# Performance work log

Hardware: AMD Instinct MI355X
Metric: run time of the kernel (lower is better)

## Reference

```python
import jax, jax.numpy as jnp
import numpy as np

B, S, D, H = 2, 2048, 1024, 16
DK = D // H
THETA = 10000.0


def apply_rope(t, pos):
    # t: [B, H, S, DK], pos: [B, S] int
    half = DK // 2
    inv_freq = THETA ** (-jnp.arange(0, DK, 2, dtype=jnp.float32) / DK)  # [half]
    ang = pos.astype(jnp.float32)[:, None, :, None] * inv_freq  # [B,1,S,half]
    cos, sin = jnp.cos(ang), jnp.sin(ang)
    t1, t2 = t[..., 0::2], t[..., 1::2]  # interleaved pairs
    r1 = t1 * cos - t2 * sin
    r2 = t1 * sin + t2 * cos
    return jnp.stack([r1, r2], axis=-1).reshape(t.shape)


def setup_inputs() -> dict:
    key = jax.random.key(0)
    ks = jax.random.split(key, 5)
    x = jax.random.normal(ks[0], (B, S, D), dtype=jnp.float32)
    scale = 0.02
    Wq = jax.random.normal(ks[1], (D, D), dtype=jnp.float32) * scale
    Wk = jax.random.normal(ks[2], (D, D), dtype=jnp.float32) * scale
    Wv = jax.random.normal(ks[3], (D, D), dtype=jnp.float32) * scale
    Wo = jax.random.normal(ks[4], (D, D), dtype=jnp.float32) * scale
    token_positions = jnp.broadcast_to(jnp.arange(S, dtype=jnp.int64), (B, S))
    return {"x": x, "Wq": Wq, "Wk": Wk, "Wv": Wv, "Wo": Wo,
            "token_positions": token_positions}


def reference(x, Wq, Wk, Wv, Wo, token_positions):
    # Bias-free linear projections: y = x @ W^T (torch Linear convention)
    q = jnp.einsum('bsd,ed->bse', x, Wq)
    k = jnp.einsum('bsd,ed->bse', x, Wk)
    v = jnp.einsum('bsd,ed->bse', x, Wv)
    # split heads: [B, S, H*DK] -> [B, H, S, DK]
    def split(t):
        return t.reshape(B, S, H, DK).transpose(0, 2, 1, 3)
    qh, kh, vh = split(q), split(k), split(v)
    qh = apply_rope(qh, token_positions)
    kh = apply_rope(kh, token_positions)
    scores = jnp.einsum('bhqd,bhkd->bhqk', qh, kh) / jnp.sqrt(jnp.float32(DK))
    causal = jnp.tril(jnp.ones((S, S), dtype=bool))
    scores = jnp.where(causal, scores, jnp.finfo(scores.dtype).min)
    probs = jax.nn.softmax(scores, axis=-1)
    out = jnp.einsum('bhqk,bhkd->bhqd', probs, vh)  # [B,H,S,DK]
    out = out.transpose(0, 2, 1, 3).reshape(B, S, D)
    return jnp.einsum('bsd,ed->bse', out, Wo)
```

## Files before the change

### kernel.cpp

```cpp
#include <hip/hip_runtime.h>
#include <stdint.h>

#define B_  2
#define S_  2048
#define D_  1024
#define H_  16
#define DK_ 64

using bf16x8 = __attribute__((ext_vector_type(8))) short;
using f32x4  = __attribute__((ext_vector_type(4))) float;

__device__ __forceinline__ unsigned short f2bf(float f) {
    union { float f; uint32_t u; } v; v.f = f;
    uint32_t r = v.u + 0x7FFFu + ((v.u >> 16) & 1u);
    return (unsigned short)(r >> 16);
}

__device__ __forceinline__ uint32_t cvtpk(float lo, float hi) {
    uint32_t r;
    asm("v_cvt_pk_bf16_f32 %0, %1, %2" : "=v"(r) : "v"(lo), "v"(hi));
    return r;
}
__device__ __forceinline__ void ps32(uint32_t& a, uint32_t& b) {
    asm volatile("v_permlane32_swap_b32 %0, %1" : "+v"(a), "+v"(b));
}
__device__ __forceinline__ void ps16(uint32_t& a, uint32_t& b) {
    asm volatile("v_permlane16_swap_b32 %0, %1" : "+v"(a), "+v"(b));
}

#define GLD16(G, L) __builtin_amdgcn_global_load_lds( \
    (const __attribute__((address_space(1))) void*)(const void*)(G), \
    (__attribute__((address_space(3))) void*)(void*)(L), 16, 0, 0)

__global__ __launch_bounds__(256) void k_f32_to_bf16(const float* __restrict__ src,
                                                     unsigned short* __restrict__ dst,
                                                     int n4) {
    int i = blockIdx.x * 256 + threadIdx.x;
    if (i >= n4) return;
    float4 v = ((const float4*)src)[i];
    union { unsigned short u[4]; uint2 d; } o;
    o.u[0] = f2bf(v.x); o.u[1] = f2bf(v.y); o.u[2] = f2bf(v.z); o.u[3] = f2bf(v.w);
    ((uint2*)dst)[i] = o.d;
}

__global__ __launch_bounds__(256) void k_wconv(
    const float* __restrict__ s0, const float* __restrict__ s1,
    const float* __restrict__ s2, const float* __restrict__ s3,
    unsigned short* __restrict__ d0, unsigned short* __restrict__ d1,
    unsigned short* __restrict__ d2, unsigned short* __restrict__ d3) {
    const int w = blockIdx.y;
    const float* s = w == 0 ? s0 : w == 1 ? s1 : w == 2 ? s2 : s3;
    unsigned short* d = w == 0 ? d0 : w == 1 ? d1 : w == 2 ? d2 : d3;
    int i = blockIdx.x * 256 + threadIdx.x;
    float4 v = ((const float4*)s)[i];
    union { unsigned short u[4]; uint2 dd; } o;
    o.u[0] = f2bf(v.x); o.u[1] = f2bf(v.y); o.u[2] = f2bf(v.z); o.u[3] = f2bf(v.w);
    ((uint2*)d)[i] = o.dd;
}

template<int MODE>
__global__ __launch_bounds__(256) void k_gemm_bt(
    const unsigned short* __restrict__ A,
    const unsigned short* __restrict__ W0,
    const unsigned short* __restrict__ W1,
    const unsigned short* __restrict__ W2,
    void* __restrict__ C0, void* __restrict__ C1, void* __restrict__ C2,
    int M, int N, int K)
{
    __shared__ __align__(16) unsigned short As[2][128 * 32];
    __shared__ __align__(16) unsigned short Bs[2][128 * 32];

    const int tid  = threadIdx.x;
    const int wid  = tid >> 6, lane = tid & 63;
    const int m16  = lane & 15, g = lane >> 4;
    const int m0   = blockIdx.x * 128, n0 = blockIdx.y * 128;
    const unsigned short* Wm = blockIdx.z == 0 ? W0 : (blockIdx.z == 1 ? W1 : W2);
    void* Cm = blockIdx.z == 0 ? C0 : (blockIdx.z == 1 ? C1 : C2);

    const int wm = (wid >> 1) * 64, wn = (wid & 1) * 64;
    const int srow = lane >> 2;
    const int scol = ((lane & 3) ^ ((lane >> 3) & 3)) * 8;
    const int sw8  = (m16 >> 1) & 3;

    const f32x4 fz = {0.f, 0.f, 0.f, 0.f};
    f32x4 acc[4][4];
#pragma unroll
    for (int i = 0; i < 4; ++i)
#pragma unroll
        for (int j = 0; j < 4; ++j) acc[i][j] = fz;

#pragma unroll
    for (int c = 0; c < 2; ++c) {
        const int chunk = wid * 2 + c;
        const int row   = chunk * 16 + srow;
        GLD16(A  + (size_t)(m0 + row) * K + scol, &As[0][chunk * 512]);
        GLD16(Wm + (size_t)(n0 + row) * K + scol, &Bs[0][chunk * 512]);
    }
    __syncthreads();

    int buf = 0;
    for (int k0 = 0; k0 < K; k0 += 32) {
        if (k0 + 32 < K) {
#pragma unroll
            for (int c = 0; c < 2; ++c) {
                const int chunk = wid * 2 + c;
                const int row   = chunk * 16 + srow;
                GLD16(A  + (size_t)(m0 + row) * K + k0 + 32 + scol, &As[buf ^ 1][chunk * 512]);
                GLD16(Wm + (size_t)(n0 + row) * K + k0 + 32 + scol, &Bs[buf ^ 1][chunk * 512]);
            }
        }
        bf16x8 af[4], bf[4];
#pragma unroll
        for (int i = 0; i < 4; ++i)
            af[i] = *(const bf16x8*)(&As[buf][(wm + i * 16 + m16) * 32 + ((g ^ sw8) * 8)]);
#pragma unroll
        for (int j = 0; j < 4; ++j)
            bf[j] = *(const bf16x8*)(&Bs[buf][(wn + j * 16 + m16) * 32 + ((g ^ sw8) * 8)]);
#pragma unroll
        for (int i = 0; i < 4; ++i)
#pragma unroll
            for (int j = 0; j < 4; ++j)
                acc[i][j] = __builtin_amdgcn_mfma_f32_16x16x32_bf16(af[i], bf[j], acc[i][j], 0, 0, 0);
        __syncthreads();
        buf ^= 1;
    }

#pragma unroll
    for (int i = 0; i < 4; ++i) {
#pragma unroll
        for (int j = 0; j < 4; ++j) {
#pragma unroll
            for (int r = 0; r < 4; ++r) {
                const int row = m0 + wm + i * 16 + g * 4 + r;
                const int col = n0 + wn + j * 16 + m16;
                const float val = acc[i][j][r];
                if (MODE == 1) {
                    ((float*)Cm)[(size_t)row * N + col] = val;
                } else {
                    const int b = row >> 11, s = row & (S_ - 1);
                    const int h = col >> 6,  dk = col & (DK_ - 1);
                    size_t idx;
                    if (blockIdx.z == 2)
                        idx = ((size_t)((b * H_ + h) * DK_ + dk)) * S_ + s;
                    else
                        idx = ((size_t)((b * H_ + h) * S_ + s)) * DK_ + dk;
                    ((unsigned short*)Cm)[idx] = f2bf(val);
                }
            }
        }
    }
}

__global__ __launch_bounds__(256) void k_rope_inplace(
    unsigned short* __restrict__ qh, unsigned short* __restrict__ kh,
    const int* __restrict__ tok)
{
    const int idx = blockIdx.x * 256 + threadIdx.x;
    const int c = idx & 7;
    const int s = (idx >> 3) & (S_ - 1);
    const int b = idx >> 18;
    const size_t off = (size_t)idx * 8;

    const float pos = (float)tok[b * S_ + s];
    float cs[4], sn[4];
#pragma unroll
    for (int i = 0; i < 4; ++i) {
        const int p = c * 4 + i;
        const float inv = exp2f((float)(-2 * p) * (13.287712379549449f / 64.f));
        sincosf(pos * inv, &sn[i], &cs[i]);
    }
    bf16x8 qv = *(bf16x8*)(qh + off);
    bf16x8 kv = *(bf16x8*)(kh + off);
    bf16x8 qo, ko;
#pragma unroll
    for (int i = 0; i < 4; ++i) {
        union { uint32_t u; float f; } q1{(uint32_t)(unsigned short)qv[2*i] << 16};
        union { uint32_t u; float f; } q2{(uint32_t)(unsigned short)qv[2*i+1] << 16};
        qo[2 * i]     = (short)f2bf(q1.f * cs[i] - q2.f * sn[i]);
        qo[2 * i + 1] = (short)f2bf(q1.f * sn[i] + q2.f * cs[i]);
        union { uint32_t u; float f; } k1{(uint32_t)(unsigned short)kv[2*i] << 16};
        union { uint32_t u; float f; } k2{(uint32_t)(unsigned short)kv[2*i+1] << 16};
        ko[2 * i]     = (short)f2bf(k1.f * cs[i] - k2.f * sn[i]);
        ko[2 * i + 1] = (short)f2bf(k1.f * sn[i] + k2.f * cs[i]);
    }
    *(bf16x8*)(qh + off) = qo;
    *(bf16x8*)(kh + off) = ko;
}

__global__ __launch_bounds__(256, 2) void k_fattn6(
    const unsigned short* __restrict__ Q,
    const unsigned short* __restrict__ K,
    const unsigned short* __restrict__ Vt,
    unsigned short* __restrict__ O)
{
    __shared__ __align__(16) unsigned short Ks[2][64 * 64];
    __shared__ __align__(16) unsigned short Vs[2][64 * 64];

    const int tid = threadIdx.x, wid = tid >> 6, lane = tid & 63;
    const int m16 = lane & 15, g = lane >> 4;
    const int bh = blockIdx.x & 31;
    const int j  = blockIdx.x >> 5;
    const int b = bh >> 4, h = bh & 15;
    const unsigned short* Qb = Q  + (size_t)bh * S_ * DK_;
    const unsigned short* Kb = K  + (size_t)bh * S_ * DK_;
    const unsigned short* Vb = Vt + (size_t)bh * DK_ * S_;

    const int r8   = lane >> 3;
    const int slot = (lane & 7) ^ r8;
    const int ch0  = wid * 2, ch1 = wid * 2 + 1;

    const f32x4 fz = {0.f, 0.f, 0.f, 0.f};
    const float kSc = 0.125f * 1.4426950408889634f;

    GLD16(Kb + (size_t)(ch0 * 8 + r8) * DK_ + slot * 8, &Ks[0][ch0 * 512]);
    GLD16(Kb + (size_t)(ch1 * 8 + r8) * DK_ + slot * 8, &Ks[0][ch1 * 512]);
    GLD16(Vb + (size_t)(ch0 * 8 + r8) * S_  + slot * 8, &Vs[0][ch0 * 512]);
    GLD16(Vb + (size_t)(ch1 * 8 + r8) * S_  + slot * 8, &Vs[0][ch1 * 512]);
    __syncthreads();

    int buf = 0;
#pragma unroll
    for (int ph = 0; ph < 2; ++ph) {
        const int qi = ph ? 31 - j : j;
        const int q0 = qi * 64;
        const int qw0 = q0 + wid * 16;

        bf16x8 qf[2];
        {
            const unsigned short* qp = Qb + (size_t)(qw0 + m16) * DK_ + g * 8;
            qf[0] = *(const bf16x8*)(qp);
            qf[1] = *(const bf16x8*)(qp + 32);
        }

        f32x4 o[4];
#pragma unroll
        for (int i = 0; i < 4; ++i) o[i] = fz;
        float ps = 0.f;

        const int nt = qi + 1;
        for (int t = 0; t < nt; ++t) {
            const int kv0 = t * 64;
            int nkv0 = -1;
            if (t + 1 < nt)      nkv0 = kv0 + 64;
            else if (ph == 0)    nkv0 = 0;
            if (nkv0 >= 0) {
                GLD16(Kb + (size_t)(nkv0 + ch0 * 8 + r8) * DK_ + slot * 8, &Ks[buf ^ 1][ch0 * 512]);
                GLD16(Kb + (size_t)(nkv0 + ch1 * 8 + r8) * DK_ + slot * 8, &Ks[buf ^ 1][ch1 * 512]);
                GLD16(Vb + (size_t)(ch0 * 8 + r8) * S_ + nkv0 + slot * 8, &Vs[buf ^ 1][ch0 * 512]);
                GLD16(Vb + (size_t)(ch1 * 8 + r8) * S_ + nkv0 + slot * 8, &Vs[buf ^ 1][ch1 * 512]);
            }

            f32x4 sc[4];
            __builtin_amdgcn_s_setprio(1);
#pragma unroll
            for (int c = 0; c < 4; ++c) {
                const int row = c * 16 + m16, rr = row & 7;
                bf16x8 kf0 = *(const bf16x8*)(&Ks[buf][row * 64 + ((g ^ rr) << 3)]);
                bf16x8 kf1 = *(const bf16x8*)(&Ks[buf][row * 64 + (((4 + g) ^ rr) << 3)]);
                f32x4 z = fz;
                z = __builtin_amdgcn_mfma_f32_16x16x32_bf16(kf0, qf[0], z, 0, 0, 0);
                z = __builtin_amdgcn_mfma_f32_16x16x32_bf16(kf1, qf[1], z, 0, 0, 0);
                sc[c] = z;
            }
            __builtin_amdgcn_s_setprio(0);

            bf16x8 vf[2][4];
#pragma unroll
            for (int c2 = 0; c2 < 4; ++c2) {
                const int rv = (c2 * 16 + m16) & 7;
                vf[0][c2] = *(const bf16x8*)(&Vs[buf][(c2 * 16 + m16) * 64 + ((g ^ rv) << 3)]);
                vf[1][c2] = *(const bf16x8*)(&Vs[buf][(c2 * 16 + m16) * 64 + (((4 + g) ^ rv) << 3)]);
            }

            const bool maskT = (t == qi);
            const int qrow = qw0 + m16;
            uint32_t pk[4][2];
#pragma unroll
            for (int c = 0; c < 4; ++c) {
                float p[4];
#pragma unroll
                for (int r = 0; r < 4; ++r) {
                    float v = exp2f(sc[c][r] * kSc);
                    if (maskT && (kv0 + c * 16 + g * 4 + r > qrow)) v = 0.f;
                    p[r] = v;
                }
                ps += (p[0] + p[1]) + (p[2] + p[3]);
                pk[c][0] = cvtpk(p[0], p[1]);
                pk[c][1] = cvtpk(p[2], p[3]);
            }

            bf16x8 pf[2];
#pragma unroll
            for (int ks = 0; ks < 2; ++ks) {
                uint32_t ylo = pk[2 * ks][0], zlo = pk[2 * ks + 1][0];
                ps32(ylo, zlo); ps16(ylo, zlo);
                uint32_t yhi = pk[2 * ks][1], zhi = pk[2 * ks + 1][1];
                ps32(yhi, zhi); ps16(yhi, zhi);
                union { uint32_t u[4]; bf16x8 v; } fu;
                fu.u[0] = ylo; fu.u[1] = yhi; fu.u[2] = zlo; fu.u[3] = zhi;
                pf[ks] = fu.v;
            }

            __builtin_amdgcn_s_setprio(1);
#pragma unroll
            for (int c2 = 0; c2 < 4; ++c2) {
                o[c2] = __builtin_amdgcn_mfma_f32_16x16x32_bf16(pf[0], vf[0][c2], o[c2], 0, 0, 0);
                o[c2] = __builtin_amdgcn_mfma_f32_16x16x32_bf16(pf[1], vf[1][c2], o[c2], 0, 0, 0);
            }
            __builtin_amdgcn_s_setprio(0);

            __syncthreads();
            buf ^= 1;
        }

        float s = ps;
        s += __shfl_xor(s, 16);
        s += __shfl_xor(s, 32);
        const float inv = 1.f / s;
        float lrq[4];
#pragma unroll
        for (int r = 0; r < 4; ++r)
            lrq[r] = __shfl(inv, g * 4 + r);
#pragma unroll
        for (int c2 = 0; c2 < 4; ++c2)
#pragma unroll
            for (int r = 0; r < 4; ++r) {
                const int orow = qw0 + g * 4 + r;
                const int ocol = h * DK_ + c2 * 16 + m16;
                O[((size_t)(b * S_ + orow)) * D_ + ocol] = f2bf(o[c2][r] * lrq[r]);
            }
    }
}

extern "C" void kernel_launch(void* const* d_in, const int* in_sizes, int n_in,
                              void* d_out, int out_size, void* d_ws, size_t ws_size,
                              hipStream_t stream) {
    (void)in_sizes; (void)n_in; (void)out_size; (void)ws_size;
    const float* x   = (const float*)d_in[0];
    const float* Wq  = (const float*)d_in[1];
    const float* Wk  = (const float*)d_in[2];
    const float* Wv  = (const float*)d_in[3];
    const float* Wo  = (const float*)d_in[4];
    const int*   tok = (const int*)d_in[5];

    char* ws = (char*)d_ws;
    const size_t MB = 1u << 20;
    unsigned short* xb  = (unsigned short*)(ws + 0 * MB);
    unsigned short* wqb = (unsigned short*)(ws + 8 * MB);
    unsigned short* wkb = (unsigned short*)(ws + 10 * MB);
    unsigned short* wvb = (unsigned short*)(ws + 12 * MB);
    unsigned short* wob = (unsigned short*)(ws + 14 * MB);
    unsigned short* qh  = (unsigned short*)(ws + 16 * MB);
    unsigned short* kh  = (unsigned short*)(ws + 24 * MB);
    unsigned short* vh  = (unsigned short*)(ws + 32 * MB);
    unsigned short* ao  = (unsigned short*)(ws + 40 * MB);

    k_f32_to_bf16<<<4096, 256, 0, stream>>>(x, xb, (B_ * S_ * D_) / 4);
    k_wconv<<<dim3(1024, 4), 256, 0, stream>>>(Wq, Wk, Wv, Wo, wqb, wkb, wvb, wob);

    k_gemm_bt<0><<<dim3(32, 8, 3), 256, 0, stream>>>(
        xb, wqb, wkb, wvb, qh, kh, vh, B_ * S_, D_, D_);

    k_rope_inplace<<<2048, 256, 0, stream>>>(qh, kh, tok);

    k_fattn6<<<dim3(512), 256, 0, stream>>>(qh, kh, vh, ao);

    k_gemm_bt<1><<<dim3(32, 8, 1), 256, 0, stream>>>(
        ao, wob, wob, wob, d_out, d_out, d_out, B_ * S_, D_, D_);
}
```

Measured before the change: 122.6 us.

## Split attention warps across query pairs and KV halves with LDS reduction

Changes the warp decomposition in the flash-attention kernel. Each pair of warps now owns 32 query rows, and each warp in the pair handles one 32-column half of every KV tile, so Q fragments and K/V fragment loads are reused across two query sub-tiles. Warps skip KV halves that lie entirely above the causal diagonal. Partial outputs and row sums are combined through shared memory before normalisation, which adds extra LDS traffic, an extra barrier and more registers per warp.

```diff
diff --git a/kernel.cpp b/kernel.cpp
--- a/kernel.cpp
+++ b/kernel.cpp
@@ -187,7 +187,7 @@
     *(bf16x8*)(kh + off) = ko;
 }
 
-__global__ __launch_bounds__(256, 2) void k_fattn6(
+__global__ __launch_bounds__(256, 2) void k_fattn7(
     const unsigned short* __restrict__ Q,
     const unsigned short* __restrict__ K,
     const unsigned short* __restrict__ Vt,
@@ -195,12 +195,16 @@
 {
     __shared__ __align__(16) unsigned short Ks[2][64 * 64];
     __shared__ __align__(16) unsigned short Vs[2][64 * 64];
+    __shared__ __align__(16) f32x4 Cx[2][8][64];
+    __shared__ float Cps[2][2][64];
 
     const int tid = threadIdx.x, wid = tid >> 6, lane = tid & 63;
     const int m16 = lane & 15, g = lane >> 4;
+    const int sub = wid >> 1;
+    const int hf  = wid & 1;
     const int bh = blockIdx.x & 31;
     const int j  = blockIdx.x >> 5;
-    const int b = bh >> 4, h = bh & 15;
+    const int b = bh >> 4, hd = bh & 15;
     const unsigned short* Qb = Q  + (size_t)bh * S_ * DK_;
     const unsigned short* Kb = K  + (size_t)bh * S_ * DK_;
     const unsigned short* Vb = Vt + (size_t)bh * DK_ * S_;
@@ -222,26 +226,27 @@
 #pragma unroll
     for (int ph = 0; ph < 2; ++ph) {
         const int qi = ph ? 31 - j : j;
-        const int q0 = qi * 64;
-        const int qw0 = q0 + wid * 16;
-
-        bf16x8 qf[2];
-        {
-            const unsigned short* qp = Qb + (size_t)(qw0 + m16) * DK_ + g * 8;
-            qf[0] = *(const bf16x8*)(qp);
-            qf[1] = *(const bf16x8*)(qp + 32);
-        }
-
-        f32x4 o[4];
-#pragma unroll
-        for (int i = 0; i < 4; ++i) o[i] = fz;
-        float ps = 0.f;
-
-        const int nt = qi + 1;
-        for (int t = 0; t < nt; ++t) {
-            const int kv0 = t * 64;
+        const int qw0 = qi * 64 + sub * 32;
+
+        bf16x8 qf[2][2];
+#pragma unroll
+        for (int mi = 0; mi < 2; ++mi) {
+            const unsigned short* qp = Qb + (size_t)(qw0 + mi * 16 + m16) * DK_ + g * 8;
+            qf[mi][0] = *(const bf16x8*)(qp);
+            qf[mi][1] = *(const bf16x8*)(qp + 32);
+        }
+
+        f32x4 o[2][4];
+#pragma unroll
+        for (int mi = 0; mi < 2; ++mi)
+#pragma unroll
+            for (int i = 0; i < 4; ++i) o[mi][i] = fz;
+        float psum[2] = {0.f, 0.f};
+
+        const int S = qi + 1;
+        for (int s = 0; s < S; ++s) {
             int nkv0 = -1;
-            if (t + 1 < nt)      nkv0 = kv0 + 64;
+            if (s + 1 < S)       nkv0 = (s + 1) * 64;
             else if (ph == 0)    nkv0 = 0;
             if (nkv0 >= 0) {
                 GLD16(Kb + (size_t)(nkv0 + ch0 * 8 + r8) * DK_ + slot * 8, &Ks[buf ^ 1][ch0 * 512]);
@@ -250,85 +255,110 @@
                 GLD16(Vb + (size_t)(ch1 * 8 + r8) * S_ + nkv0 + slot * 8, &Vs[buf ^ 1][ch1 * 512]);
             }
 
-            f32x4 sc[4];
-            __builtin_amdgcn_s_setprio(1);
-#pragma unroll
-            for (int c = 0; c < 4; ++c) {
-                const int row = c * 16 + m16, rr = row & 7;
-                bf16x8 kf0 = *(const bf16x8*)(&Ks[buf][row * 64 + ((g ^ rr) << 3)]);
-                bf16x8 kf1 = *(const bf16x8*)(&Ks[buf][row * 64 + (((4 + g) ^ rr) << 3)]);
-                f32x4 z = fz;
-                z = __builtin_amdgcn_mfma_f32_16x16x32_bf16(kf0, qf[0], z, 0, 0, 0);
-                z = __builtin_amdgcn_mfma_f32_16x16x32_bf16(kf1, qf[1], z, 0, 0, 0);
-                sc[c] = z;
+            const int kvb = s * 64 + hf * 32;
+            if (kvb <= qw0 + 31) {
+                bf16x8 kf[2][2];
+#pragma unroll
+                for (int cc = 0; cc < 2; ++cc) {
+                    const int row = (2 * hf + cc) * 16 + m16, rr = row & 7;
+                    kf[cc][0] = *(const bf16x8*)(&Ks[buf][row * 64 + ((g ^ rr) << 3)]);
+                    kf[cc][1] = *(const bf16x8*)(&Ks[buf][row * 64 + (((4 + g) ^ rr) << 3)]);
+                }
+                f32x4 sc[2][2];
+                __builtin_amdgcn_s_setprio(1);
+#pragma unroll
+                for (int cc = 0; cc < 2; ++cc)
+#pragma unroll
+                    for (int mi = 0; mi < 2; ++mi) {
+                        f32x4 z = fz;
+                        z = __builtin_amdgcn_mfma_f32_16x16x32_bf16(kf[cc][0], qf[mi][0], z, 0, 0, 0);
+                        z = __builtin_amdgcn_mfma_f32_16x16x32_bf16(kf[cc][1], qf[mi][1], z, 0, 0, 0);
+                        sc[mi][cc] = z;
+                    }
+                __builtin_amdgcn_s_setprio(0);
+
+                bf16x8 vf[4];
+#pragma unroll
+                for (int c2 = 0; c2 < 4; ++c2) {
+                    const int dv = c2 * 16 + m16, rv = dv & 7;
+                    vf[c2] = *(const bf16x8*)(&Vs[buf][dv * 64 + (((4 * hf + g) ^ rv) << 3)]);
+                }
+
+                bf16x8 pf[2];
+#pragma unroll
+                for (int mi = 0; mi < 2; ++mi) {
+                    const int qrow = qw0 + mi * 16 + m16;
+                    const bool maskT = (kvb + 31 > qw0 + mi * 16);
+                    uint32_t pkc[2][2];
+#pragma unroll
+                    for (int cc = 0; cc < 2; ++cc) {
+                        float p[4];
+#pragma unroll
+                        for (int r = 0; r < 4; ++r) {
+                            float v = exp2f(sc[mi][cc][r] * kSc);
+                            if (maskT && (kvb + cc * 16 + g * 4 + r > qrow)) v = 0.f;
+                            p[r] = v;
+                        }
+                        psum[mi] += (p[0] + p[1]) + (p[2] + p[3]);
+                        pkc[cc][0] = cvtpk(p[0], p[1]);
+                        pkc[cc][1] = cvtpk(p[2], p[3]);
+                    }
+                    uint32_t ylo = pkc[0][0], zlo = pkc[1][0];
+                    ps32(ylo, zlo); ps16(ylo, zlo);
+                    uint32_t yhi = pkc[0][1], zhi = pkc[1][1];
+                    ps32(yhi, zhi); ps16(yhi, zhi);
+                    union { uint32_t u[4]; bf16x8 v; } fu;
+                    fu.u[0] = ylo; fu.u[1] = yhi; fu.u[2] = zlo; fu.u[3] = zhi;
+                    pf[mi] = fu.v;
+                }
+
+                __builtin_amdgcn_s_setprio(1);
+#pragma unroll
+                for (int mi = 0; mi < 2; ++mi)
+#pragma unroll
+                    for (int c2 = 0; c2 < 4; ++c2)
+                        o[mi][c2] = __builtin_amdgcn_mfma_f32_16x16x32_bf16(pf[mi], vf[c2], o[mi][c2], 0, 0, 0);
+                __builtin_amdgcn_s_setprio(0);
             }
-            __builtin_amdgcn_s_setprio(0);
-
-            bf16x8 vf[2][4];
-#pragma unroll
-            for (int c2 = 0; c2 < 4; ++c2) {
-                const int rv = (c2 * 16 + m16) & 7;
-                vf[0][c2] = *(const bf16x8*)(&Vs[buf][(c2 * 16 + m16) * 64 + ((g ^ rv) << 3)]);
-                vf[1][c2] = *(const bf16x8*)(&Vs[buf][(c2 * 16 + m16) * 64 + (((4 + g) ^ rv) << 3)]);
-            }
-
-            const bool maskT = (t == qi);
-            const int qrow = qw0 + m16;
-            uint32_t pk[4][2];
-#pragma unroll
-            for (int c = 0; c < 4; ++c) {
-                float p[4];
-#pragma unroll
-                for (int r = 0; r < 4; ++r) {
-                    float v = exp2f(sc[c][r] * kSc);
-                    if (maskT && (kv0 + c * 16 + g * 4 + r > qrow)) v = 0.f;
-                    p[r] = v;
-                }
-                ps += (p[0] + p[1]) + (p[2] + p[3]);
-                pk[c][0] = cvtpk(p[0], p[1]);
-                pk[c][1] = cvtpk(p[2], p[3]);
-            }
-
-            bf16x8 pf[2];
-#pragma unroll
-            for (int ks = 0; ks < 2; ++ks) {
-                uint32_t ylo = pk[2 * ks][0], zlo = pk[2 * ks + 1][0];
-                ps32(ylo, zlo); ps16(ylo, zlo);
-                uint32_t yhi = pk[2 * ks][1], zhi = pk[2 * ks + 1][1];
-                ps32(yhi, zhi); ps16(yhi, zhi);
-                union { uint32_t u[4]; bf16x8 v; } fu;
-                fu.u[0] = ylo; fu.u[1] = yhi; fu.u[2] = zlo; fu.u[3] = zhi;
-                pf[ks] = fu.v;
-            }
-
-            __builtin_amdgcn_s_setprio(1);
-#pragma unroll
-            for (int c2 = 0; c2 < 4; ++c2) {
-                o[c2] = __builtin_amdgcn_mfma_f32_16x16x32_bf16(pf[0], vf[0][c2], o[c2], 0, 0, 0);
-                o[c2] = __builtin_amdgcn_mfma_f32_16x16x32_bf16(pf[1], vf[1][c2], o[c2], 0, 0, 0);
-            }
-            __builtin_amdgcn_s_setprio(0);
-
             __syncthreads();
             buf ^= 1;
         }
 
-        float s = ps;
-        s += __shfl_xor(s, 16);
-        s += __shfl_xor(s, 32);
-        const float inv = 1.f / s;
-        float lrq[4];
-#pragma unroll
-        for (int r = 0; r < 4; ++r)
-            lrq[r] = __shfl(inv, g * 4 + r);
-#pragma unroll
-        for (int c2 = 0; c2 < 4; ++c2)
-#pragma unroll
-            for (int r = 0; r < 4; ++r) {
-                const int orow = qw0 + g * 4 + r;
-                const int ocol = h * DK_ + c2 * 16 + m16;
-                O[((size_t)(b * S_ + orow)) * D_ + ocol] = f2bf(o[c2][r] * lrq[r]);
+        if (hf == 1) {
+#pragma unroll
+            for (int mi = 0; mi < 2; ++mi)
+#pragma unroll
+                for (int c2 = 0; c2 < 4; ++c2)
+                    Cx[sub][mi * 4 + c2][lane] = o[mi][c2];
+            Cps[sub][0][lane] = psum[0];
+            Cps[sub][1][lane] = psum[1];
+        }
+        __syncthreads();
+        if (hf == 0) {
+#pragma unroll
+            for (int mi = 0; mi < 2; ++mi) {
+#pragma unroll
+                for (int c2 = 0; c2 < 4; ++c2)
+                    o[mi][c2] += Cx[sub][mi * 4 + c2][lane];
+                float ssum = psum[mi] + Cps[sub][mi][lane];
+                ssum += __shfl_xor(ssum, 16);
+                ssum += __shfl_xor(ssum, 32);
+                const float inv = 1.f / ssum;
+                float lrq[4];
+#pragma unroll
+                for (int r = 0; r < 4; ++r)
+                    lrq[r] = __shfl(inv, g * 4 + r);
+#pragma unroll
+                for (int c2 = 0; c2 < 4; ++c2)
+#pragma unroll
+                    for (int r = 0; r < 4; ++r) {
+                        const int orow = qw0 + mi * 16 + g * 4 + r;
+                        const int ocol = hd * DK_ + c2 * 16 + m16;
+                        O[((size_t)(b * S_ + orow)) * D_ + ocol] = f2bf(o[mi][c2][r] * lrq[r]);
+                    }
             }
+        }
+        __syncthreads();
     }
 }
 
@@ -363,7 +393,7 @@
 
     k_rope_inplace<<<2048, 256, 0, stream>>>(qh, kh, tok);
 
-    k_fattn6<<<dim3(512), 256, 0, stream>>>(qh, kh, vh, ao);
+    k_fattn7<<<dim3(512), 256, 0, stream>>>(qh, kh, vh, ao);
 
     k_gemm_bt<1><<<dim3(32, 8, 1), 256, 0, stream>>>(
         ao, wob, wob, wob, d_out, d_out, d_out, B_ * S_, D_, D_);
```

After: 127.3 us. +3.8%, slower.

## Triple-buffer K/V tiles and fuse both causal phases into one flat loop

Applied to the files above, without the earlier changes.

The attention kernel now keeps three LDS buffers for K/V tiles and prefetches two tiles ahead. It replaces the two-phase nested loop with a single 33-iteration loop that handles both the low and high query tiles, flushing the first output partway through. A single barrier per iteration, placed after an explicit vmcnt wait, replaces the trailing __syncthreads, so the load for the next tile can overlap compute. In exchange, LDS use grows by half, which may limit occupancy, and the manual waitcnt counts must exactly match the number of outstanding loads.

```diff
diff --git a/kernel.cpp b/kernel.cpp
--- a/kernel.cpp
+++ b/kernel.cpp
@@ -187,14 +187,14 @@
     *(bf16x8*)(kh + off) = ko;
 }
 
-__global__ __launch_bounds__(256, 2) void k_fattn6(
+__global__ __launch_bounds__(256, 2) void k_fattn8(
     const unsigned short* __restrict__ Q,
     const unsigned short* __restrict__ K,
     const unsigned short* __restrict__ Vt,
     unsigned short* __restrict__ O)
 {
-    __shared__ __align__(16) unsigned short Ks[2][64 * 64];
-    __shared__ __align__(16) unsigned short Vs[2][64 * 64];
+    __shared__ __align__(16) unsigned short Ks[3][64 * 64];
+    __shared__ __align__(16) unsigned short Vs[3][64 * 64];
 
     const int tid = threadIdx.x, wid = tid >> 6, lane = tid & 63;
     const int m16 = lane & 15, g = lane >> 4;
@@ -211,108 +211,146 @@
 
     const f32x4 fz = {0.f, 0.f, 0.f, 0.f};
     const float kSc = 0.125f * 1.4426950408889634f;
-
-    GLD16(Kb + (size_t)(ch0 * 8 + r8) * DK_ + slot * 8, &Ks[0][ch0 * 512]);
-    GLD16(Kb + (size_t)(ch1 * 8 + r8) * DK_ + slot * 8, &Ks[0][ch1 * 512]);
-    GLD16(Vb + (size_t)(ch0 * 8 + r8) * S_  + slot * 8, &Vs[0][ch0 * 512]);
-    GLD16(Vb + (size_t)(ch1 * 8 + r8) * S_  + slot * 8, &Vs[0][ch1 * 512]);
-    __syncthreads();
-
-    int buf = 0;
-#pragma unroll
-    for (int ph = 0; ph < 2; ++ph) {
-        const int qi = ph ? 31 - j : j;
-        const int q0 = qi * 64;
-        const int qw0 = q0 + wid * 16;
-
-        bf16x8 qf[2];
-        {
-            const unsigned short* qp = Qb + (size_t)(qw0 + m16) * DK_ + g * 8;
-            qf[0] = *(const bf16x8*)(qp);
-            qf[1] = *(const bf16x8*)(qp + 32);
-        }
-
-        f32x4 o[4];
-#pragma unroll
-        for (int i = 0; i < 4; ++i) o[i] = fz;
-        float ps = 0.f;
-
-        const int nt = qi + 1;
-        for (int t = 0; t < nt; ++t) {
-            const int kv0 = t * 64;
-            int nkv0 = -1;
-            if (t + 1 < nt)      nkv0 = kv0 + 64;
-            else if (ph == 0)    nkv0 = 0;
-            if (nkv0 >= 0) {
-                GLD16(Kb + (size_t)(nkv0 + ch0 * 8 + r8) * DK_ + slot * 8, &Ks[buf ^ 1][ch0 * 512]);
-                GLD16(Kb + (size_t)(nkv0 + ch1 * 8 + r8) * DK_ + slot * 8, &Ks[buf ^ 1][ch1 * 512]);
-                GLD16(Vb + (size_t)(ch0 * 8 + r8) * S_ + nkv0 + slot * 8, &Vs[buf ^ 1][ch0 * 512]);
-                GLD16(Vb + (size_t)(ch1 * 8 + r8) * S_ + nkv0 + slot * 8, &Vs[buf ^ 1][ch1 * 512]);
+    const int nt0 = j + 1;
+
+    const int qrow0 = j * 64 + wid * 16 + m16;
+    const int qrow1 = (31 - j) * 64 + wid * 16 + m16;
+    bf16x8 qf0[2], qf1[2];
+    {
+        const unsigned short* qp = Qb + (size_t)qrow0 * DK_ + g * 8;
+        qf0[0] = *(const bf16x8*)(qp);
+        qf0[1] = *(const bf16x8*)(qp + 32);
+    }
+    {
+        const unsigned short* qp = Qb + (size_t)qrow1 * DK_ + g * 8;
+        qf1[0] = *(const bf16x8*)(qp);
+        qf1[1] = *(const bf16x8*)(qp + 32);
+    }
+
+    {
+        GLD16(Kb + (size_t)(ch0 * 8 + r8) * DK_ + slot * 8, &Ks[0][ch0 * 512]);
+        GLD16(Kb + (size_t)(ch1 * 8 + r8) * DK_ + slot * 8, &Ks[0][ch1 * 512]);
+        GLD16(Vb + (size_t)(ch0 * 8 + r8) * S_  + slot * 8, &Vs[0][ch0 * 512]);
+        GLD16(Vb + (size_t)(ch1 * 8 + r8) * S_  + slot * 8, &Vs[0][ch1 * 512]);
+        const int kv1 = (1 < nt0 ? 1 : 0) * 64;
+        GLD16(Kb + (size_t)(kv1 + ch0 * 8 + r8) * DK_ + slot * 8, &Ks[1][ch0 * 512]);
+        GLD16(Kb + (size_t)(kv1 + ch1 * 8 + r8) * DK_ + slot * 8, &Ks[1][ch1 * 512]);
+        GLD16(Vb + (size_t)(ch0 * 8 + r8) * S_ + kv1 + slot * 8, &Vs[1][ch0 * 512]);
+        GLD16(Vb + (size_t)(ch1 * 8 + r8) * S_ + kv1 + slot * 8, &Vs[1][ch1 * 512]);
+    }
+
+    f32x4 o[4];
+#pragma unroll
+    for (int i = 0; i < 4; ++i) o[i] = fz;
+    float ps = 0.f;
+
+    for (int u = 0; u < 33; ++u) {
+        const int phase = (u >= nt0) ? 1 : 0;
+
+        if (u == nt0) {
+            float s = ps;
+            s += __shfl_xor(s, 16);
+            s += __shfl_xor(s, 32);
+            const float inv = 1.f / s;
+            float lrq[4];
+#pragma unroll
+            for (int r = 0; r < 4; ++r)
+                lrq[r] = __shfl(inv, g * 4 + r);
+#pragma unroll
+            for (int c2 = 0; c2 < 4; ++c2)
+#pragma unroll
+                for (int r = 0; r < 4; ++r) {
+                    const int orow = j * 64 + wid * 16 + g * 4 + r;
+                    const int ocol = h * DK_ + c2 * 16 + m16;
+                    O[((size_t)(b * S_ + orow)) * D_ + ocol] = f2bf(o[c2][r] * lrq[r]);
+                }
+#pragma unroll
+            for (int i = 0; i < 4; ++i) o[i] = fz;
+            ps = 0.f;
+        }
+
+        if (u < 32) asm volatile("s_waitcnt vmcnt(4)" ::: "memory");
+        else        asm volatile("s_waitcnt vmcnt(0)" ::: "memory");
+        __builtin_amdgcn_s_barrier();
+        __builtin_amdgcn_sched_barrier(0);
+
+        if (u + 2 < 33) {
+            const int v2 = u + 2;
+            const int kv2 = (v2 < nt0 ? v2 : v2 - nt0) * 64;
+            unsigned short* kd = &Ks[(u + 2) % 3][0];
+            unsigned short* vd = &Vs[(u + 2) % 3][0];
+            GLD16(Kb + (size_t)(kv2 + ch0 * 8 + r8) * DK_ + slot * 8, kd + ch0 * 512);
+            GLD16(Kb + (size_t)(kv2 + ch1 * 8 + r8) * DK_ + slot * 8, kd + ch1 * 512);
+            GLD16(Vb + (size_t)(ch0 * 8 + r8) * S_ + kv2 + slot * 8, vd + ch0 * 512);
+            GLD16(Vb + (size_t)(ch1 * 8 + r8) * S_ + kv2 + slot * 8, vd + ch1 * 512);
+        }
+
+        const int kv0 = (phase ? u - nt0 : u) * 64;
+        const unsigned short* Kbuf = &Ks[u % 3][0];
+        const unsigned short* Vbuf = &Vs[u % 3][0];
+        const bf16x8* qf = phase ? qf1 : qf0;
+        const int qrow = phase ? qrow1 : qrow0;
+
+        f32x4 sc[4];
+        __builtin_amdgcn_s_setprio(1);
+#pragma unroll
+        for (int c = 0; c < 4; ++c) {
+            const int row = c * 16 + m16, rr = row & 7;
+            bf16x8 kf0 = *(const bf16x8*)(Kbuf + row * 64 + ((g ^ rr) << 3));
+            bf16x8 kf1 = *(const bf16x8*)(Kbuf + row * 64 + (((4 + g) ^ rr) << 3));
+            f32x4 z = fz;
+            z = __builtin_amdgcn_mfma_f32_16x16x32_bf16(kf0, qf[0], z, 0, 0, 0);
+            z = __builtin_amdgcn_mfma_f32_16x16x32_bf16(kf1, qf[1], z, 0, 0, 0);
+            sc[c] = z;
+        }
+        __builtin_amdgcn_s_setprio(0);
+
+        bf16x8 vf[2][4];
+#pragma unroll
+        for (int c2 = 0; c2 < 4; ++c2) {
+            const int rv = (c2 * 16 + m16) & 7;
+            vf[0][c2] = *(const bf16x8*)(Vbuf + (c2 * 16 + m16) * 64 + ((g ^ rv) << 3));
+            vf[1][c2] = *(const bf16x8*)(Vbuf + (c2 * 16 + m16) * 64 + (((4 + g) ^ rv) << 3));
+        }
+
+        const bool maskT = (u == nt0 - 1) || (u == 32);
+        uint32_t pk[4][2];
+#pragma unroll
+        for (int c = 0; c < 4; ++c) {
+            float p[4];
+#pragma unroll
+            for (int r = 0; r < 4; ++r) {
+                float v = exp2f(sc[c][r] * kSc);
+                if (maskT && (kv0 + c * 16 + g * 4 + r > qrow)) v = 0.f;
+                p[r] = v;
             }
-
-            f32x4 sc[4];
-            __builtin_amdgcn_s_setprio(1);
-#pragma unroll
-            for (int c = 0; c < 4; ++c) {
-                const int row = c * 16 + m16, rr = row & 7;
-                bf16x8 kf0 = *(const bf16x8*)(&Ks[buf][row * 64 + ((g ^ rr) << 3)]);
-                bf16x8 kf1 = *(const bf16x8*)(&Ks[buf][row * 64 + (((4 + g) ^ rr) << 3)]);
-                f32x4 z = fz;
-                z = __builtin_amdgcn_mfma_f32_16x16x32_bf16(kf0, qf[0], z, 0, 0, 0);
-                z = __builtin_amdgcn_mfma_f32_16x16x32_bf16(kf1, qf[1], z, 0, 0, 0);
-                sc[c] = z;
-            }
-            __builtin_amdgcn_s_setprio(0);
-
-            bf16x8 vf[2][4];
-#pragma unroll
-            for (int c2 = 0; c2 < 4; ++c2) {
-                const int rv = (c2 * 16 + m16) & 7;
-                vf[0][c2] = *(const bf16x8*)(&Vs[buf][(c2 * 16 + m16) * 64 + ((g ^ rv) << 3)]);
-                vf[1][c2] = *(const bf16x8*)(&Vs[buf][(c2 * 16 + m16) * 64 + (((4 + g) ^ rv) << 3)]);
-            }
-
-            const bool maskT = (t == qi);
-            const int qrow = qw0 + m16;
-            uint32_t pk[4][2];
-#pragma unroll
-            for (int c = 0; c < 4; ++c) {
-                float p[4];
-#pragma unroll
-                for (int r = 0; r < 4; ++r) {
-                    float v = exp2f(sc[c][r] * kSc);
-                    if (maskT && (kv0 + c * 16 + g * 4 + r > qrow)) v = 0.f;
-                    p[r] = v;
-                }
-                ps += (p[0] + p[1]) + (p[2] + p[3]);
-                pk[c][0] = cvtpk(p[0], p[1]);
-                pk[c][1] = cvtpk(p[2], p[3]);
-            }
-
-            bf16x8 pf[2];
-#pragma unroll
-            for (int ks = 0; ks < 2; ++ks) {
-                uint32_t ylo = pk[2 * ks][0], zlo = pk[2 * ks + 1][0];
-                ps32(ylo, zlo); ps16(ylo, zlo);
-                uint32_t yhi = pk[2 * ks][1], zhi = pk[2 * ks + 1][1];
-                ps32(yhi, zhi); ps16(yhi, zhi);
-                union { uint32_t u[4]; bf16x8 v; } fu;
-                fu.u[0] = ylo; fu.u[1] = yhi; fu.u[2] = zlo; fu.u[3] = zhi;
-                pf[ks] = fu.v;
-            }
-
-            __builtin_amdgcn_s_setprio(1);
-#pragma unroll
-            for (int c2 = 0; c2 < 4; ++c2) {
-                o[c2] = __builtin_amdgcn_mfma_f32_16x16x32_bf16(pf[0], vf[0][c2], o[c2], 0, 0, 0);
-                o[c2] = __builtin_amdgcn_mfma_f32_16x16x32_bf16(pf[1], vf[1][c2], o[c2], 0, 0, 0);
-            }
-            __builtin_amdgcn_s_setprio(0);
-
-            __syncthreads();
-            buf ^= 1;
-        }
-
+            ps += (p[0] + p[1]) + (p[2] + p[3]);
+            pk[c][0] = cvtpk(p[0], p[1]);
+            pk[c][1] = cvtpk(p[2], p[3]);
+        }
+
+        bf16x8 pf[2];
+#pragma unroll
+        for (int ks = 0; ks < 2; ++ks) {
+            uint32_t ylo = pk[2 * ks][0], zlo = pk[2 * ks + 1][0];
+            ps32(ylo, zlo); ps16(ylo, zlo);
+            uint32_t yhi = pk[2 * ks][1], zhi = pk[2 * ks + 1][1];
+            ps32(yhi, zhi); ps16(yhi, zhi);
+            union { uint32_t u[4]; bf16x8 v; } fu;
+            fu.u[0] = ylo; fu.u[1] = yhi; fu.u[2] = zlo; fu.u[3] = zhi;
+            pf[ks] = fu.v;
+        }
+
+        __builtin_amdgcn_s_setprio(1);
+#pragma unroll
+        for (int c2 = 0; c2 < 4; ++c2) {
+            o[c2] = __builtin_amdgcn_mfma_f32_16x16x32_bf16(pf[0], vf[0][c2], o[c2], 0, 0, 0);
+            o[c2] = __builtin_amdgcn_mfma_f32_16x16x32_bf16(pf[1], vf[1][c2], o[c2], 0, 0, 0);
+        }
+        __builtin_amdgcn_s_setprio(0);
+    }
+
+    {
         float s = ps;
         s += __shfl_xor(s, 16);
         s += __shfl_xor(s, 32);
@@ -325,7 +363,7 @@
         for (int c2 = 0; c2 < 4; ++c2)
 #pragma unroll
             for (int r = 0; r < 4; ++r) {
-                const int orow = qw0 + g * 4 + r;
+                const int orow = (31 - j) * 64 + wid * 16 + g * 4 + r;
                 const int ocol = h * DK_ + c2 * 16 + m16;
                 O[((size_t)(b * S_ + orow)) * D_ + ocol] = f2bf(o[c2][r] * lrq[r]);
             }
@@ -363,7 +401,7 @@
 
     k_rope_inplace<<<2048, 256, 0, stream>>>(qh, kh, tok);
 
-    k_fattn6<<<dim3(512), 256, 0, stream>>>(qh, kh, vh, ao);
+    k_fattn8<<<dim3(512), 256, 0, stream>>>(qh, kh, vh, ao);
 
     k_gemm_bt<1><<<dim3(32, 8, 1), 256, 0, stream>>>(
         ao, wob, wob, wob, d_out, d_out, d_out, B_ * S_, D_, D_);
```

Measured after the change: 128.4 us. 4.8% more time.

## Process two 64-key tiles per barrier in flash attention with 128-wide staging

Applied to the files above, without the earlier changes.

The attention kernel now stages 128 keys of K and V per double-buffered step and computes two 64-key tiles between each barrier, halving the number of __syncthreads and global-load issue rounds. The V staging layout and its swizzle change to a 128-wide row. Shared memory per block doubles to 64 KB, which may limit how many blocks fit per CU. Odd tile counts are handled by skipping the second tile.

```diff
diff --git a/kernel.cpp b/kernel.cpp
--- a/kernel.cpp
+++ b/kernel.cpp
@@ -187,14 +187,81 @@
     *(bf16x8*)(kh + off) = ko;
 }
 
-__global__ __launch_bounds__(256, 2) void k_fattn6(
+#define TILE_PF(T, diag, kvb, pfOut)                                         \
+  {                                                                          \
+    f32x4 sc_[4];                                                            \
+    __builtin_amdgcn_s_setprio(1);                                           \
+    _Pragma("unroll")                                                        \
+    for (int c = 0; c < 4; ++c) {                                            \
+      const int row_ = (T) * 64 + c * 16 + m16, rr_ = row_ & 7;              \
+      bf16x8 kf0 = *(const bf16x8*)(Kbuf + row_ * 64 + ((g ^ rr_) << 3));    \
+      bf16x8 kf1 = *(const bf16x8*)(Kbuf + row_ * 64 + (((4 + g) ^ rr_) << 3)); \
+      f32x4 z_ = fz;                                                         \
+      z_ = __builtin_amdgcn_mfma_f32_16x16x32_bf16(kf0, qf[0], z_, 0, 0, 0); \
+      z_ = __builtin_amdgcn_mfma_f32_16x16x32_bf16(kf1, qf[1], z_, 0, 0, 0); \
+      sc_[c] = z_;                                                           \
+    }                                                                        \
+    __builtin_amdgcn_s_setprio(0);                                           \
+    uint32_t pk_[4][2];                                                      \
+    _Pragma("unroll")                                                        \
+    for (int c = 0; c < 4; ++c) {                                            \
+      float p_[4];                                                           \
+      _Pragma("unroll")                                                      \
+      for (int r = 0; r < 4; ++r) {                                          \
+        float v_ = exp2f(sc_[c][r] * kSc);                                   \
+        if ((diag) && ((kvb) + c * 16 + g * 4 + r > qrow)) v_ = 0.f;         \
+        p_[r] = v_;                                                          \
+      }                                                                      \
+      ps += (p_[0] + p_[1]) + (p_[2] + p_[3]);                               \
+      pk_[c][0] = cvtpk(p_[0], p_[1]);                                       \
+      pk_[c][1] = cvtpk(p_[2], p_[3]);                                       \
+    }                                                                        \
+    _Pragma("unroll")                                                        \
+    for (int ks = 0; ks < 2; ++ks) {                                         \
+      uint32_t ylo = pk_[2 * ks][0], zlo = pk_[2 * ks + 1][0];               \
+      ps32(ylo, zlo); ps16(ylo, zlo);                                        \
+      uint32_t yhi = pk_[2 * ks][1], zhi = pk_[2 * ks + 1][1];               \
+      ps32(yhi, zhi); ps16(yhi, zhi);                                        \
+      union { uint32_t u[4]; bf16x8 v; } fu_;                                \
+      fu_.u[0] = ylo; fu_.u[1] = yhi; fu_.u[2] = zlo; fu_.u[3] = zhi;        \
+      pfOut[ks] = fu_.v;                                                     \
+    }                                                                        \
+  }
+
+#define TILE_PV(T, pfIn)                                                     \
+  {                                                                          \
+    __builtin_amdgcn_s_setprio(1);                                           \
+    _Pragma("unroll")                                                        \
+    for (int c2 = 0; c2 < 4; ++c2) {                                         \
+      const int dv_ = c2 * 16 + m16, rv_ = dv_ & 7;                          \
+      bf16x8 v0 = *(const bf16x8*)(Vbuf + dv_ * 128 + ((((T) * 8 + g) ^ rv_) << 3)); \
+      bf16x8 v1 = *(const bf16x8*)(Vbuf + dv_ * 128 + ((((T) * 8 + 4 + g) ^ rv_) << 3)); \
+      o[c2] = __builtin_amdgcn_mfma_f32_16x16x32_bf16(pfIn[0], v0, o[c2], 0, 0, 0); \
+      o[c2] = __builtin_amdgcn_mfma_f32_16x16x32_bf16(pfIn[1], v1, o[c2], 0, 0, 0); \
+    }                                                                        \
+    __builtin_amdgcn_s_setprio(0);                                           \
+  }
+
+#define STAGE_KV(bd, kb)                                                     \
+  {                                                                          \
+    _Pragma("unroll")                                                        \
+    for (int c = 0; c < 4; ++c) {                                            \
+      const int chunk_ = wid * 4 + c;                                        \
+      const int krow_ = chunk_ * 8 + kr8;                                    \
+      GLD16(Kb + (size_t)((kb) + krow_) * DK_ + kslot * 8, &Ks[bd][chunk_ * 512]); \
+      const int dv_ = chunk_ * 4 + vr4;                                      \
+      GLD16(Vb + (size_t)dv_ * S_ + (kb) + ((vs0 ^ (dv_ & 7)) * 8), &Vs[bd][chunk_ * 512]); \
+    }                                                                        \
+  }
+
+__global__ __launch_bounds__(256, 2) void k_fattn9(
     const unsigned short* __restrict__ Q,
     const unsigned short* __restrict__ K,
     const unsigned short* __restrict__ Vt,
     unsigned short* __restrict__ O)
 {
-    __shared__ __align__(16) unsigned short Ks[2][64 * 64];
-    __shared__ __align__(16) unsigned short Vs[2][64 * 64];
+    __shared__ __align__(16) unsigned short Ks[2][128 * 64];
+    __shared__ __align__(16) unsigned short Vs[2][64 * 128];
 
     const int tid = threadIdx.x, wid = tid >> 6, lane = tid & 63;
     const int m16 = lane & 15, g = lane >> 4;
@@ -205,29 +272,27 @@
     const unsigned short* Kb = K  + (size_t)bh * S_ * DK_;
     const unsigned short* Vb = Vt + (size_t)bh * DK_ * S_;
 
-    const int r8   = lane >> 3;
-    const int slot = (lane & 7) ^ r8;
-    const int ch0  = wid * 2, ch1 = wid * 2 + 1;
+    const int kr8 = lane >> 3;
+    const int kslot = (lane & 7) ^ kr8;
+    const int vr4 = lane >> 4;
+    const int vs0 = lane & 15;
 
     const f32x4 fz = {0.f, 0.f, 0.f, 0.f};
     const float kSc = 0.125f * 1.4426950408889634f;
 
-    GLD16(Kb + (size_t)(ch0 * 8 + r8) * DK_ + slot * 8, &Ks[0][ch0 * 512]);
-    GLD16(Kb + (size_t)(ch1 * 8 + r8) * DK_ + slot * 8, &Ks[0][ch1 * 512]);
-    GLD16(Vb + (size_t)(ch0 * 8 + r8) * S_  + slot * 8, &Vs[0][ch0 * 512]);
-    GLD16(Vb + (size_t)(ch1 * 8 + r8) * S_  + slot * 8, &Vs[0][ch1 * 512]);
+    STAGE_KV(0, 0)
     __syncthreads();
 
     int buf = 0;
 #pragma unroll
     for (int ph = 0; ph < 2; ++ph) {
         const int qi = ph ? 31 - j : j;
-        const int q0 = qi * 64;
-        const int qw0 = q0 + wid * 16;
+        const int qw0 = qi * 64 + wid * 16;
+        const int qrow = qw0 + m16;
 
         bf16x8 qf[2];
         {
-            const unsigned short* qp = Qb + (size_t)(qw0 + m16) * DK_ + g * 8;
+            const unsigned short* qp = Qb + (size_t)qrow * DK_ + g * 8;
             qf[0] = *(const bf16x8*)(qp);
             qf[1] = *(const bf16x8*)(qp + 32);
         }
@@ -238,76 +303,25 @@
         float ps = 0.f;
 
         const int nt = qi + 1;
-        for (int t = 0; t < nt; ++t) {
-            const int kv0 = t * 64;
-            int nkv0 = -1;
-            if (t + 1 < nt)      nkv0 = kv0 + 64;
-            else if (ph == 0)    nkv0 = 0;
-            if (nkv0 >= 0) {
-                GLD16(Kb + (size_t)(nkv0 + ch0 * 8 + r8) * DK_ + slot * 8, &Ks[buf ^ 1][ch0 * 512]);
-                GLD16(Kb + (size_t)(nkv0 + ch1 * 8 + r8) * DK_ + slot * 8, &Ks[buf ^ 1][ch1 * 512]);
-                GLD16(Vb + (size_t)(ch0 * 8 + r8) * S_ + nkv0 + slot * 8, &Vs[buf ^ 1][ch0 * 512]);
-                GLD16(Vb + (size_t)(ch1 * 8 + r8) * S_ + nkv0 + slot * 8, &Vs[buf ^ 1][ch1 * 512]);
-            }
-
-            f32x4 sc[4];
-            __builtin_amdgcn_s_setprio(1);
-#pragma unroll
-            for (int c = 0; c < 4; ++c) {
-                const int row = c * 16 + m16, rr = row & 7;
-                bf16x8 kf0 = *(const bf16x8*)(&Ks[buf][row * 64 + ((g ^ rr) << 3)]);
-                bf16x8 kf1 = *(const bf16x8*)(&Ks[buf][row * 64 + (((4 + g) ^ rr) << 3)]);
-                f32x4 z = fz;
-                z = __builtin_amdgcn_mfma_f32_16x16x32_bf16(kf0, qf[0], z, 0, 0, 0);
-                z = __builtin_amdgcn_mfma_f32_16x16x32_bf16(kf1, qf[1], z, 0, 0, 0);
-                sc[c] = z;
-            }
-            __builtin_amdgcn_s_setprio(0);
-
-            bf16x8 vf[2][4];
-#pragma unroll
-            for (int c2 = 0; c2 < 4; ++c2) {
-                const int rv = (c2 * 16 + m16) & 7;
-                vf[0][c2] = *(const bf16x8*)(&Vs[buf][(c2 * 16 + m16) * 64 + ((g ^ rv) << 3)]);
-                vf[1][c2] = *(const bf16x8*)(&Vs[buf][(c2 * 16 + m16) * 64 + (((4 + g) ^ rv) << 3)]);
-            }
-
-            const bool maskT = (t == qi);
-            const int qrow = qw0 + m16;
-            uint32_t pk[4][2];
-#pragma unroll
-            for (int c = 0; c < 4; ++c) {
-                float p[4];
-#pragma unroll
-                for (int r = 0; r < 4; ++r) {
-                    float v = exp2f(sc[c][r] * kSc);
-                    if (maskT && (kv0 + c * 16 + g * 4 + r > qrow)) v = 0.f;
-                    p[r] = v;
-                }
-                ps += (p[0] + p[1]) + (p[2] + p[3]);
-                pk[c][0] = cvtpk(p[0], p[1]);
-                pk[c][1] = cvtpk(p[2], p[3]);
-            }
-
-            bf16x8 pf[2];
-#pragma unroll
-            for (int ks = 0; ks < 2; ++ks) {
-                uint32_t ylo = pk[2 * ks][0], zlo = pk[2 * ks + 1][0];
-                ps32(ylo, zlo); ps16(ylo, zlo);
-                uint32_t yhi = pk[2 * ks][1], zhi = pk[2 * ks + 1][1];
-                ps32(yhi, zhi); ps16(yhi, zhi);
-                union { uint32_t u[4]; bf16x8 v; } fu;
-                fu.u[0] = ylo; fu.u[1] = yhi; fu.u[2] = zlo; fu.u[3] = zhi;
-                pf[ks] = fu.v;
-            }
-
-            __builtin_amdgcn_s_setprio(1);
-#pragma unroll
-            for (int c2 = 0; c2 < 4; ++c2) {
-                o[c2] = __builtin_amdgcn_mfma_f32_16x16x32_bf16(pf[0], vf[0][c2], o[c2], 0, 0, 0);
-                o[c2] = __builtin_amdgcn_mfma_f32_16x16x32_bf16(pf[1], vf[1][c2], o[c2], 0, 0, 0);
-            }
-            __builtin_amdgcn_s_setprio(0);
+        const int nI = (nt + 1) >> 1;
+        for (int i = 0; i < nI; ++i) {
+            int nkb = -1;
+            if (i + 1 < nI)      nkb = (i + 1) * 128;
+            else if (ph == 0)    nkb = 0;
+            if (nkb >= 0) STAGE_KV(buf ^ 1, nkb)
+
+            const unsigned short* Kbuf = Ks[buf];
+            const unsigned short* Vbuf = Vs[buf];
+            const int kbA = i * 128;
+            const bool vB = (2 * i + 1 < nt);
+            const bool dA = (2 * i == nt - 1);
+            const bool dB = (2 * i + 1 == nt - 1);
+
+            bf16x8 pfA[2], pfB[2];
+            TILE_PF(0, dA, kbA, pfA)
+            if (vB) { TILE_PF(1, dB, kbA + 64, pfB) }
+            TILE_PV(0, pfA)
+            if (vB) { TILE_PV(1, pfB) }
 
             __syncthreads();
             buf ^= 1;
@@ -363,7 +377,7 @@
 
     k_rope_inplace<<<2048, 256, 0, stream>>>(qh, kh, tok);
 
-    k_fattn6<<<dim3(512), 256, 0, stream>>>(qh, kh, vh, ao);
+    k_fattn9<<<dim3(512), 256, 0, stream>>>(qh, kh, vh, ao);
 
     k_gemm_bt<1><<<dim3(32, 8, 1), 256, 0, stream>>>(
         ao, wob, wob, wob, d_out, d_out, d_out, B_ * S_, D_, D_);
```

Measured after the change: 127.0 us. 1.04x slower.
